# Performance work log

Hardware: AMD Instinct MI355X
Metric: run time of the kernel (lower is better)

## Reference

```python
import jax, jax.numpy as jnp
import numpy as np

B, C, H, W = 16, 1, 1024, 1024


def _filters():
    fx = jnp.array([[0, 0, 0.0], [1, -2, 1], [0, 0, 0]], dtype=jnp.float32)
    fy = jnp.array([[0, 1, 0.0], [0, -2, 0], [0, 1, 0]], dtype=jnp.float32)
    fd1 = jnp.array([[1, 0, 0.0], [0, -2, 0], [0, 0, 1]], dtype=jnp.float32)
    fd2 = jnp.array([[0, 0, 1.0], [0, -2, 0], [1, 0, 0]], dtype=jnp.float32)
    return jnp.stack([fx, fy, fd1, fd2])[:, None, :, :]  # [4,1,3,3] OIHW


def _masks(h, w):
    # mask_x: last column zero; mask_y: last row zero; mask_diag: all borders zero
    mx = jnp.ones((h, w), jnp.float32).at[:, -1].set(0.0)
    my = jnp.ones((h, w), jnp.float32).at[-1, :].set(0.0)
    md = jnp.zeros((h, w), jnp.float32).at[1:-1, 1:-1].set(1.0)
    return jnp.stack([mx, my, md, md])[None]  # [1,4,h,w], broadcasts over batch


def _grads(x, filt):
    # 3x3 stencil conv, padding=1, stride=1: [B,1,H,W] -> [B,4,H,W]
    return jax.lax.conv_general_dilated(
        x, filt, window_strides=(1, 1), padding=((1, 1), (1, 1)),
        dimension_numbers=('NCHW', 'OIHW', 'NCHW'))


def _smooth_l1(d):
    ad = jnp.abs(d)
    return jnp.where(ad < 1.0, 0.5 * d * d, ad - 0.5)


def setup_inputs() -> dict:
    key = jax.random.key(0)
    k1, k2 = jax.random.split(key)
    return {
        'input': jax.random.normal(k1, (B, C, H, W), dtype=jnp.float32),
        'target': jax.random.normal(k2, (B, C, H, W), dtype=jnp.float32),
    }


def reference(input, target):
    filt = _filters()
    masks = _masks(input.shape[2], input.shape[3])
    gi = _grads(input, filt)
    gt = _grads(target, filt)
    diff = _smooth_l1(gi - gt)
    return jnp.mean(diff * masks)
```

## Files before the change

### kernel.cpp

```cpp
#include <hip/hip_runtime.h>


#define BB 16
#define HH 1024
#define WW 1024
#define RR 8

__device__ __forceinline__ float sl1(float v) {
  float ad = fabsf(v);
  float t = fminf(ad, 1.0f);
  return fmaf(0.5f * t, t, ad - t);
}

__global__ __launch_bounds__(256) void smooth_partial(
    const float* __restrict__ in, const float* __restrict__ tg,
    float* __restrict__ ws) {
  const int tid  = threadIdx.x;
  const int lane = tid & 63;
  const int wave = tid >> 6;
  const int x0   = tid * 4;
  const int strip = blockIdx.x;
  const int bi = strip >> 7;
  const int r0 = (strip & 127) * RR;
  const int imgBase = bi * (HH * WW);

  float4 a4[RR + 2], b4[RR + 2];
  #pragma unroll
  for (int k = 0; k < RR + 2; ++k) {
    const int y = r0 - 1 + k;
    if (y >= 0 && y < HH) {
      const int base = imgBase + y * WW + x0;
      a4[k] = *reinterpret_cast<const float4*>(in + base);
      b4[k] = *reinterpret_cast<const float4*>(tg + base);
    } else {
      a4[k] = make_float4(0.f, 0.f, 0.f, 0.f);
      b4[k] = make_float4(0.f, 0.f, 0.f, 0.f);
    }
  }
  __builtin_amdgcn_sched_barrier(0);

  float4 Dc[RR + 2];
  float  Dl[RR + 2], Dr[RR + 2];
  __shared__ float shL[4][RR + 2];
  __shared__ float shR[4][RR + 2];

  #pragma unroll
  for (int k = 0; k < RR + 2; ++k) {
    Dc[k].x = a4[k].x - b4[k].x;
    Dc[k].y = a4[k].y - b4[k].y;
    Dc[k].z = a4[k].z - b4[k].z;
    Dc[k].w = a4[k].w - b4[k].w;
    Dl[k] = __shfl_up(Dc[k].w, 1, 64);
    Dr[k] = __shfl_down(Dc[k].x, 1, 64);
    if (lane == 63) shL[wave][k] = Dc[k].w;
    if (lane == 0)  shR[wave][k] = Dc[k].x;
  }
  __syncthreads();
  #pragma unroll
  for (int k = 0; k < RR + 2; ++k) {
    if (lane == 0)  Dl[k] = (wave > 0) ? shL[wave - 1][k] : 0.f;
    if (lane == 63) Dr[k] = (wave < 3) ? shR[wave + 1][k] : 0.f;
  }

  float sum = 0.f;
  #pragma unroll
  for (int k = 0; k < RR; ++k) {
    const int y = r0 + k;
    const float my  = (y == HH - 1) ? 0.f : 1.f;
    const float mdy = (y == 0 || y == HH - 1) ? 0.f : 1.f;
    const float P[6] = {Dl[k  ], Dc[k  ].x, Dc[k  ].y, Dc[k  ].z, Dc[k  ].w, Dr[k  ]};
    const float C[6] = {Dl[k+1], Dc[k+1].x, Dc[k+1].y, Dc[k+1].z, Dc[k+1].w, Dr[k+1]};
    const float N[6] = {Dl[k+2], Dc[k+2].x, Dc[k+2].y, Dc[k+2].z, Dc[k+2].w, Dr[k+2]};
    #pragma unroll
    for (int j = 1; j <= 4; ++j) {
      const int x = x0 + j - 1;
      const float c2 = -2.f * C[j];
      const float fx = (C[j-1] + C[j+1]) + c2;
      const float fy = (P[j]   + N[j]  ) + c2;
      const float f1 = (P[j-1] + N[j+1]) + c2;
      const float f2 = (P[j+1] + N[j-1]) + c2;
      const float mx  = (x == WW - 1) ? 0.f : 1.f;
      const float mdx = (x == 0 || x == WW - 1) ? 0.f : 1.f;
      sum += sl1(fx) * mx + sl1(fy) * my + (sl1(f1) + sl1(f2)) * (mdx * mdy);
    }
  }

  for (int off = 32; off > 0; off >>= 1) sum += __shfl_down(sum, off, 64);
  __shared__ float sh[4];
  if (lane == 0) sh[wave] = sum;
  __syncthreads();
  if (tid == 0) ws[blockIdx.x] = (sh[0] + sh[1]) + (sh[2] + sh[3]);
}

__global__ __launch_bounds__(256) void smooth_final(
    const float* __restrict__ ws, float* __restrict__ out, int n) {
  float s = 0.f;
  for (int i = threadIdx.x; i < n; i += 256) s += ws[i];
  for (int off = 32; off > 0; off >>= 1) s += __shfl_down(s, off, 64);
  __shared__ float sh[4];
  const int wave = threadIdx.x >> 6, lane = threadIdx.x & 63;
  if (lane == 0) sh[wave] = s;
  __syncthreads();
  if (threadIdx.x == 0) {
    const float scale = 1.0f / (float)((long long)BB * 4LL * HH * WW);
    out[0] = ((sh[0] + sh[1]) + (sh[2] + sh[3])) * scale;
  }
}

extern "C" void kernel_launch(void* const* d_in, const int* in_sizes, int n_in,
                              void* d_out, int out_size, void* d_ws, size_t ws_size,
                              hipStream_t stream) {
  const float* in = (const float*)d_in[0];
  const float* tg = (const float*)d_in[1];
  float* out = (float*)d_out;
  float* ws  = (float*)d_ws;

  const int nblocks = BB * (HH / RR);
  smooth_partial<<<nblocks, 256, 0, stream>>>(in, tg, ws);
  smooth_final<<<1, 256, 0, stream>>>(ws, out, nblocks);
}
```

Baseline: 36.93 us.

## Stage input rows through LDS with direct global-to-LDS loads

Input and target row loads now use global_load_lds, which writes directly into a shared-memory tile of RR+2 rows per tensor, instead of going through registers. Rows are then read back from LDS one at a time with a rolling previous/current/next window. Halo columns at wave edges are read straight from LDS, replacing the old shared exchange. The goal is lower register pressure and higher occupancy, at the cost of about 80KB of LDS per block, which may itself limit how many blocks fit on a CU, plus an extra LDS read pass.

```diff
diff --git a/kernel.cpp b/kernel.cpp
--- a/kernel.cpp
+++ b/kernel.cpp
@@ -5,6 +5,9 @@
 #define HH 1024
 #define WW 1024
 #define RR 8
+
+typedef __attribute__((address_space(1))) const void GVoid;
+typedef __attribute__((address_space(3))) void LVoid;
 
 __device__ __forceinline__ float sl1(float v) {
   float ad = fabsf(v);
@@ -15,6 +18,10 @@
 __global__ __launch_bounds__(256) void smooth_partial(
     const float* __restrict__ in, const float* __restrict__ tg,
     float* __restrict__ ws) {
+  __shared__ __align__(16) float As[RR + 2][WW];
+  __shared__ __align__(16) float Bs[RR + 2][WW];
+  __shared__ float shred[4];
+
   const int tid  = threadIdx.x;
   const int lane = tid & 63;
   const int wave = tid >> 6;
@@ -22,55 +29,50 @@
   const int strip = blockIdx.x;
   const int bi = strip >> 7;
   const int r0 = (strip & 127) * RR;
-  const int imgBase = bi * (HH * WW);
+  const size_t imgBase = (size_t)bi * HH * WW;
 
-  float4 a4[RR + 2], b4[RR + 2];
   #pragma unroll
   for (int k = 0; k < RR + 2; ++k) {
     const int y = r0 - 1 + k;
     if (y >= 0 && y < HH) {
-      const int base = imgBase + y * WW + x0;
-      a4[k] = *reinterpret_cast<const float4*>(in + base);
-      b4[k] = *reinterpret_cast<const float4*>(tg + base);
+      const float* ga = in + imgBase + (size_t)y * WW + x0;
+      const float* gb = tg + imgBase + (size_t)y * WW + x0;
+      __builtin_amdgcn_global_load_lds((GVoid*)ga, (LVoid*)&As[k][wave * 256], 16, 0, 0);
+      __builtin_amdgcn_global_load_lds((GVoid*)gb, (LVoid*)&Bs[k][wave * 256], 16, 0, 0);
     } else {
-      a4[k] = make_float4(0.f, 0.f, 0.f, 0.f);
-      b4[k] = make_float4(0.f, 0.f, 0.f, 0.f);
+      const float4 z = make_float4(0.f, 0.f, 0.f, 0.f);
+      *reinterpret_cast<float4*>(&As[k][x0]) = z;
+      *reinterpret_cast<float4*>(&Bs[k][x0]) = z;
     }
   }
-  __builtin_amdgcn_sched_barrier(0);
+  asm volatile("s_waitcnt vmcnt(0)" ::: "memory");
+  __syncthreads();
 
-  float4 Dc[RR + 2];
-  float  Dl[RR + 2], Dr[RR + 2];
-  __shared__ float shL[4][RR + 2];
-  __shared__ float shR[4][RR + 2];
+  auto loadD = [&](int k, float4& C, float& L, float& R) {
+    const float4 a = *reinterpret_cast<const float4*>(&As[k][x0]);
+    const float4 b = *reinterpret_cast<const float4*>(&Bs[k][x0]);
+    C.x = a.x - b.x; C.y = a.y - b.y; C.z = a.z - b.z; C.w = a.w - b.w;
+    L = __shfl_up(C.w, 1, 64);
+    R = __shfl_down(C.x, 1, 64);
+    if (lane == 0)  L = (tid > 0)   ? As[k][x0 - 1] - Bs[k][x0 - 1] : 0.f;
+    if (lane == 63) R = (tid < 255) ? As[k][x0 + 4] - Bs[k][x0 + 4] : 0.f;
+  };
 
-  #pragma unroll
-  for (int k = 0; k < RR + 2; ++k) {
-    Dc[k].x = a4[k].x - b4[k].x;
-    Dc[k].y = a4[k].y - b4[k].y;
-    Dc[k].z = a4[k].z - b4[k].z;
-    Dc[k].w = a4[k].w - b4[k].w;
-    Dl[k] = __shfl_up(Dc[k].w, 1, 64);
-    Dr[k] = __shfl_down(Dc[k].x, 1, 64);
-    if (lane == 63) shL[wave][k] = Dc[k].w;
-    if (lane == 0)  shR[wave][k] = Dc[k].x;
-  }
-  __syncthreads();
-  #pragma unroll
-  for (int k = 0; k < RR + 2; ++k) {
-    if (lane == 0)  Dl[k] = (wave > 0) ? shL[wave - 1][k] : 0.f;
-    if (lane == 63) Dr[k] = (wave < 3) ? shR[wave + 1][k] : 0.f;
-  }
+  float4 Pc, Cc, Nc;
+  float  Pl, Pr, Cl, Cr, Nl, Nr;
+  loadD(0, Pc, Pl, Pr);
+  loadD(1, Cc, Cl, Cr);
 
   float sum = 0.f;
   #pragma unroll
   for (int k = 0; k < RR; ++k) {
     const int y = r0 + k;
+    loadD(k + 2, Nc, Nl, Nr);
     const float my  = (y == HH - 1) ? 0.f : 1.f;
     const float mdy = (y == 0 || y == HH - 1) ? 0.f : 1.f;
-    const float P[6] = {Dl[k  ], Dc[k  ].x, Dc[k  ].y, Dc[k  ].z, Dc[k  ].w, Dr[k  ]};
-    const float C[6] = {Dl[k+1], Dc[k+1].x, Dc[k+1].y, Dc[k+1].z, Dc[k+1].w, Dr[k+1]};
-    const float N[6] = {Dl[k+2], Dc[k+2].x, Dc[k+2].y, Dc[k+2].z, Dc[k+2].w, Dr[k+2]};
+    const float P[6] = {Pl, Pc.x, Pc.y, Pc.z, Pc.w, Pr};
+    const float C[6] = {Cl, Cc.x, Cc.y, Cc.z, Cc.w, Cr};
+    const float N[6] = {Nl, Nc.x, Nc.y, Nc.z, Nc.w, Nr};
     #pragma unroll
     for (int j = 1; j <= 4; ++j) {
       const int x = x0 + j - 1;
@@ -83,13 +85,14 @@
       const float mdx = (x == 0 || x == WW - 1) ? 0.f : 1.f;
       sum += sl1(fx) * mx + sl1(fy) * my + (sl1(f1) + sl1(f2)) * (mdx * mdy);
     }
+    Pl = Cl; Pr = Cr; Pc = Cc;
+    Cl = Nl; Cr = Nr; Cc = Nc;
   }
 
   for (int off = 32; off > 0; off >>= 1) sum += __shfl_down(sum, off, 64);
-  __shared__ float sh[4];
-  if (lane == 0) sh[wave] = sum;
+  if (lane == 0) shred[wave] = sum;
   __syncthreads();
-  if (tid == 0) ws[blockIdx.x] = (sh[0] + sh[1]) + (sh[2] + sh[3]);
+  if (tid == 0) ws[blockIdx.x] = (shred[0] + shred[1]) + (shred[2] + shred[3]);
 }
 
 __global__ __launch_bounds__(256) void smooth_final(
```

New measurement: 58.23 us. 57.6% more time.
